# Performance work log

Measured on AMD Instinct MI355X. Metric: run time of the kernel, lower is better.

The kernel has to match this reference:

```python
import jax, jax.numpy as jnp
import numpy as np

N = 50000
D = 128
E = 600000


def setup_inputs() -> dict:
    key = jax.random.key(0)
    k1, k2, k3, k4, k5, k6 = jax.random.split(key, 6)
    x = jax.random.normal(k1, (N, D), dtype=jnp.float32)
    edge_index = jax.random.randint(k2, (2, E), 0, N, dtype=jnp.int32)
    s = 1.0 / np.sqrt(D)
    W1 = jax.random.uniform(k3, (D, D), dtype=jnp.float32, minval=-s, maxval=s)
    b1 = jax.random.uniform(k4, (D,), dtype=jnp.float32, minval=-s, maxval=s)
    W2 = jax.random.uniform(k5, (D, D), dtype=jnp.float32, minval=-s, maxval=s)
    b2 = jax.random.uniform(k6, (D,), dtype=jnp.float32, minval=-s, maxval=s)
    return {"x": x, "edge_index": edge_index, "W1": W1, "b1": b1, "W2": W2, "b2": b2}


def _gcn_conv(x, src, dst, W, b):
    # PyG GCNConv (default flow source->target): out[dst] += norm * (x @ W)[src] + b
    n = x.shape[0]
    deg = jax.ops.segment_sum(jnp.ones_like(dst, dtype=x.dtype), dst, num_segments=n)
    dinv = jnp.where(deg > 0, jax.lax.rsqrt(deg), 0.0)
    norm = dinv[src] * dinv[dst]          # [E+N]
    h = x @ W                             # [N, D]
    msg = h[src] * norm[:, None]          # [E+N, D] gather + scale
    out = jax.ops.segment_sum(msg, dst, num_segments=n)
    return out + b


def reference(x, edge_index, W1, b1, W2, b2):
    n = x.shape[0]
    loops = jnp.arange(n, dtype=edge_index.dtype)
    src = jnp.concatenate([edge_index[0], loops])  # add self-loops
    dst = jnp.concatenate([edge_index[1], loops])
    h = jax.nn.relu(_gcn_conv(x, src, dst, W1, b1))
    out = jax.nn.relu(_gcn_conv(h, src, dst, W2, b2))
    return out
```

## Files before the change

kernel.cpp:

```cpp
#include <hip/hip_runtime.h>
#include <stdint.h>

typedef __attribute__((ext_vector_type(8))) short bf16x8;
typedef __attribute__((ext_vector_type(4))) float f32x4;

#define CAP 64

__device__ __forceinline__ float bf2f(unsigned int u) {
    union { unsigned int i; float f; } v; v.i = u << 16; return v.f;
}
__device__ __forceinline__ unsigned int f2bf(float f) {
    union { float f; unsigned int i; } v; v.f = f;
    unsigned int b = v.i;
    b += 0x7FFFu + ((b >> 16) & 1u);
    return b >> 16;
}


__global__ void bucket_kernel(const int* __restrict__ src, const int* __restrict__ dst,
                              int* __restrict__ counts, unsigned short* __restrict__ bucket,
                              int E,
                              const float* __restrict__ W1, const float* __restrict__ W2,
                              unsigned short* __restrict__ Wt1, unsigned short* __restrict__ Wt2) {
    int t = blockIdx.x * 256 + threadIdx.x;
    if (t < 32768) {
        const float* W = (t < 16384) ? W1 : W2;
        unsigned short* O = (t < 16384) ? Wt1 : Wt2;
        int i = t & 16383;
        O[i] = (unsigned short)f2bf(W[(i & 127) * 128 + (i >> 7)]);
    }
    if (t < E) {
        int s = src[t], d = dst[t];
        int slot = atomicAdd(&counts[d], 1);
        if (slot < CAP - 1) bucket[(size_t)d * CAP + slot + 1] = (unsigned short)s;
    }
}


__global__ __launch_bounds__(256) void gemm128(const float* __restrict__ A,
                                               const unsigned short* __restrict__ Wt,
                                               const int* __restrict__ counts,
                                               unsigned short* __restrict__ bucket,
                                               unsigned short* __restrict__ G, int M) {
    int t = threadIdx.x;
    int wave = t >> 6, lane = t & 63;
    int mrow = lane & 15, quad = lane >> 4;

    {
        int row = blockIdx.x * 64 + (t >> 2);
        if (row < M) {
            int rows = 1 + min(counts[row], CAP - 1);
            int pe = (rows + 15) & ~15;
            if ((t & 3) == 0) bucket[(size_t)row * CAP] = (unsigned short)row;
            for (int idx = rows + (t & 3); idx < pe; idx += 4)
                bucket[(size_t)row * CAP + idx] = (unsigned short)M;
        }
    }
    if (blockIdx.x == 0 && t < 64)
        ((unsigned int*)G)[(size_t)M * 64 + t] = 0u;

    int m0 = (blockIdx.x * 4 + wave) * 16;
    int arow = m0 + mrow;
    int srow = arow < M ? arow : M - 1;
    const float* Arow = A + (size_t)srow * 128;

    f32x4 acc[8];
#pragma unroll
    for (int nt = 0; nt < 8; ++nt) acc[nt] = (f32x4){0.f, 0.f, 0.f, 0.f};

#pragma unroll
    for (int kb = 0; kb < 4; ++kb) {
        f32x4 lo = *(const f32x4*)(Arow + kb * 32 + quad * 8);
        f32x4 hi = *(const f32x4*)(Arow + kb * 32 + quad * 8 + 4);
        bf16x8 a;
#pragma unroll
        for (int i = 0; i < 4; ++i) { a[i] = (short)f2bf(lo[i]); a[i + 4] = (short)f2bf(hi[i]); }
#pragma unroll
        for (int nt = 0; nt < 8; ++nt) {
            bf16x8 b = *(const bf16x8*)(Wt + (size_t)(nt * 16 + mrow) * 128 + kb * 32 + quad * 8);
            acc[nt] = __builtin_amdgcn_mfma_f32_16x16x32_bf16(a, b, acc[nt], 0, 0, 0);
        }
    }

#pragma unroll
    for (int r = 0; r < 4; ++r) {
        int row = m0 + quad * 4 + r;
        if (row < M) {
            float dr = rsqrtf((float)counts[row] + 1.0f);
#pragma unroll
            for (int nt = 0; nt < 8; ++nt)
                G[(size_t)row * 128 + nt * 16 + mrow] = (unsigned short)f2bf(acc[nt][r] * dr);
        }
    }
}


template <bool FINAL>
__global__ __launch_bounds__(256) void agg_kernel(const unsigned short* __restrict__ g,
                                                  const int* __restrict__ counts,
                                                  const unsigned short* __restrict__ bucket,
                                                  const float* __restrict__ bias,
                                                  const unsigned short* __restrict__ Wt,
                                                  unsigned short* __restrict__ G2,
                                                  float* __restrict__ outf,
                                                  int N) {
    __shared__ __align__(16) unsigned short As[FINAL ? 1 : 16][136];
    int wave = threadIdx.x >> 6, lane = threadIdx.x & 63;
    int p = lane & 15, grp = lane >> 4;
    const char* gb = (const char*)g;
    int nb0 = blockIdx.x * 16 + wave * 4;

    if (!FINAL && blockIdx.x == 0 && threadIdx.x < 64)
        ((unsigned int*)G2)[(size_t)N * 64 + threadIdx.x] = 0u;

    float4 bva = ((const float4*)bias)[p * 2];
    float4 bvb = ((const float4*)bias)[p * 2 + 1];

    int degs[4]; unsigned int svs[4];
#pragma unroll
    for (int i = 0; i < 4; ++i) {
        int n = min(nb0 + i, N - 1);
        degs[i] = counts[n];
        svs[i]  = bucket[(size_t)n * CAP + lane];
    }

    uint4 vq[4][4];
#pragma unroll
    for (int i = 0; i < 4; ++i)
#pragma unroll
        for (int q = 0; q < 4; ++q) {
            int s = __shfl((int)svs[i], 4 * q + grp);
            vq[i][q] = *(const uint4*)(gb + (size_t)s * 256 + p * 16);
        }

#pragma unroll
    for (int i = 0; i < 4; ++i) {
        int deg = degs[i];
        int rows = 1 + min(deg, CAP - 1);
        int mr = (rows + 15) & ~15;
        float di = rsqrtf((float)deg + 1.0f);
        float acc[8];
#pragma unroll
        for (int k = 0; k < 8; ++k) acc[k] = 0.f;
#pragma unroll
        for (int q = 0; q < 4; ++q)
#pragma unroll
            for (int d = 0; d < 4; ++d) {
                unsigned int v = (&vq[i][q].x)[d];
                acc[d * 2]     += bf2f(v & 0xFFFFu);
                acc[d * 2 + 1] += bf2f(v >> 16);
            }
#pragma unroll 1
        for (int j0 = 16; j0 < mr; j0 += 16) {
            uint4 tq[4];
#pragma unroll
            for (int q = 0; q < 4; ++q) {
                int s = __shfl((int)svs[i], j0 + 4 * q + grp);
                tq[q] = *(const uint4*)(gb + (size_t)s * 256 + p * 16);
            }
#pragma unroll
            for (int q = 0; q < 4; ++q)
#pragma unroll
                for (int d = 0; d < 4; ++d) {
                    unsigned int v = (&tq[q].x)[d];
                    acc[d * 2]     += bf2f(v & 0xFFFFu);
                    acc[d * 2 + 1] += bf2f(v >> 16);
                }
        }
#pragma unroll
        for (int k = 0; k < 8; ++k) {
            acc[k] += __shfl_xor(acc[k], 16);
            acc[k] += __shfl_xor(acc[k], 32);
        }
        float o[8];
        o[0] = fmaxf(acc[0] * di + bva.x, 0.f);
        o[1] = fmaxf(acc[1] * di + bva.y, 0.f);
        o[2] = fmaxf(acc[2] * di + bva.z, 0.f);
        o[3] = fmaxf(acc[3] * di + bva.w, 0.f);
        o[4] = fmaxf(acc[4] * di + bvb.x, 0.f);
        o[5] = fmaxf(acc[5] * di + bvb.y, 0.f);
        o[6] = fmaxf(acc[6] * di + bvb.z, 0.f);
        o[7] = fmaxf(acc[7] * di + bvb.w, 0.f);

        if (FINAL) {
            if (grp == i) {
                int n = nb0 + i;
                if (n < N) {
                    float4* op = (float4*)(outf + (size_t)n * 128 + p * 8);
                    op[0] = make_float4(o[0], o[1], o[2], o[3]);
                    op[1] = make_float4(o[4], o[5], o[6], o[7]);
                }
            }
        } else {
            if (grp == i) {
                uint4 w;
                w.x = f2bf(o[0]) | (f2bf(o[1]) << 16);
                w.y = f2bf(o[2]) | (f2bf(o[3]) << 16);
                w.z = f2bf(o[4]) | (f2bf(o[5]) << 16);
                w.w = f2bf(o[6]) | (f2bf(o[7]) << 16);
                *(uint4*)&As[wave * 4 + i][p * 8] = w;
            }
        }
    }

    if (FINAL) return;

    __syncthreads();

    int mrow = lane & 15, quad = lane >> 4;
    f32x4 acc2[2];
    acc2[0] = (f32x4){0.f, 0.f, 0.f, 0.f};
    acc2[1] = (f32x4){0.f, 0.f, 0.f, 0.f};
#pragma unroll
    for (int kb = 0; kb < 4; ++kb) {
        bf16x8 a = *(const bf16x8*)(&As[mrow][kb * 32 + quad * 8]);
#pragma unroll
        for (int q = 0; q < 2; ++q) {
            int nt = wave * 2 + q;
            bf16x8 b = *(const bf16x8*)(Wt + (size_t)(nt * 16 + mrow) * 128 + kb * 32 + quad * 8);
            acc2[q] = __builtin_amdgcn_mfma_f32_16x16x32_bf16(a, b, acc2[q], 0, 0, 0);
        }
    }
#pragma unroll
    for (int r = 0; r < 4; ++r) {
        int row = blockIdx.x * 16 + quad * 4 + r;
        if (row < N) {
            float dr = rsqrtf((float)counts[row] + 1.0f);
#pragma unroll
            for (int q = 0; q < 2; ++q) {
                int nt = wave * 2 + q;
                G2[(size_t)row * 128 + nt * 16 + mrow] = (unsigned short)f2bf(acc2[q][r] * dr);
            }
        }
    }
}


extern "C" void kernel_launch(void* const* d_in, const int* in_sizes, int n_in,
                              void* d_out, int out_size, void* d_ws, size_t ws_size,
                              hipStream_t stream) {
    const float* x  = (const float*)d_in[0];
    const int*   ei = (const int*)d_in[1];
    const float* W1 = (const float*)d_in[2];
    const float* b1 = (const float*)d_in[3];
    const float* W2 = (const float*)d_in[4];
    const float* b2 = (const float*)d_in[5];
    float* out = (float*)d_out;

    int N = in_sizes[0] / 128;
    int E = in_sizes[1] / 2;
    const int* src = ei;
    const int* dst = ei + E;

    char* p = (char*)d_ws;
    auto alloc = [&](size_t bytes) {
        char* r = p; p += (bytes + 255) & ~(size_t)255; return r;
    };
    int*            counts = (int*)           alloc((size_t)N * 4);
    unsigned short* bucket = (unsigned short*)alloc((size_t)N * CAP * 2);
    unsigned short* g1     = (unsigned short*)alloc((size_t)(N + 1) * 128 * 2);
    unsigned short* g2     = (unsigned short*)alloc((size_t)(N + 1) * 128 * 2);
    unsigned short* Wt1    = (unsigned short*)alloc(16384 * 2);
    unsigned short* Wt2    = (unsigned short*)alloc(16384 * 2);

    hipMemsetAsync(counts, 0, (size_t)N * 4, stream);
    bucket_kernel<<<(E + 255) / 256, 256, 0, stream>>>(src, dst, counts, bucket, E,
                                                       W1, W2, Wt1, Wt2);

    gemm128<<<(N + 63) / 64, 256, 0, stream>>>(x, Wt1, counts, bucket, g1, N);
    agg_kernel<false><<<(N + 15) / 16, 256, 0, stream>>>(g1, counts, bucket, b1, Wt2, g2, nullptr, N);
    agg_kernel<true ><<<(N + 15) / 16, 256, 0, stream>>>(g2, counts, bucket, b2, nullptr, nullptr, out, N);
}
```

Before: 194.5 us.

## Replace global-atomic bucketing with range-partitioned LDS atomic bucket scan

Edge indices are first compacted to 16-bit arrays. Then 256 blocks each scan the whole compacted edge list and bucket only the destinations that fall in their own node range, using shared-memory atomics instead of global atomics. This removes the memset and the contended global atomics, and moves bucket padding out of the GEMM. In exchange every block rereads the full 1.2 MB destination array, which is 256 times the edge traffic, although most of it should hit in L2.

```diff
diff --git a/kernel.cpp b/kernel.cpp
--- a/kernel.cpp
+++ b/kernel.cpp
@@ -3,8 +3,10 @@
 
 typedef __attribute__((ext_vector_type(8))) short bf16x8;
 typedef __attribute__((ext_vector_type(4))) float f32x4;
+typedef __attribute__((ext_vector_type(8))) unsigned short u16x8;
 
 #define CAP 64
+#define SCAN_BLOCKS 256
 
 __device__ __forceinline__ float bf2f(unsigned int u) {
     union { unsigned int i; float f; } v; v.i = u << 16; return v.f;
@@ -17,11 +19,15 @@
 }
 
 
-__global__ void bucket_kernel(const int* __restrict__ src, const int* __restrict__ dst,
-                              int* __restrict__ counts, unsigned short* __restrict__ bucket,
-                              int E,
-                              const float* __restrict__ W1, const float* __restrict__ W2,
-                              unsigned short* __restrict__ Wt1, unsigned short* __restrict__ Wt2) {
+__global__ __launch_bounds__(256) void compact_kernel(const int* __restrict__ src,
+                                                      const int* __restrict__ dst,
+                                                      int E, int Epad,
+                                                      unsigned short* __restrict__ s16,
+                                                      unsigned short* __restrict__ d16,
+                                                      const float* __restrict__ W1,
+                                                      const float* __restrict__ W2,
+                                                      unsigned short* __restrict__ Wt1,
+                                                      unsigned short* __restrict__ Wt2) {
     int t = blockIdx.x * 256 + threadIdx.x;
     if (t < 32768) {
         const float* W = (t < 16384) ? W1 : W2;
@@ -29,10 +35,71 @@
         int i = t & 16383;
         O[i] = (unsigned short)f2bf(W[(i & 127) * 128 + (i >> 7)]);
     }
-    if (t < E) {
-        int s = src[t], d = dst[t];
-        int slot = atomicAdd(&counts[d], 1);
-        if (slot < CAP - 1) bucket[(size_t)d * CAP + slot + 1] = (unsigned short)s;
+    int e0 = t * 8;
+    if (e0 < Epad) {
+        u16x8 sv, dv;
+        if (e0 + 8 <= E) {
+            int4 a0 = *(const int4*)(src + e0), a1 = *(const int4*)(src + e0 + 4);
+            int4 b0 = *(const int4*)(dst + e0), b1 = *(const int4*)(dst + e0 + 4);
+            sv[0]=(unsigned short)a0.x; sv[1]=(unsigned short)a0.y; sv[2]=(unsigned short)a0.z; sv[3]=(unsigned short)a0.w;
+            sv[4]=(unsigned short)a1.x; sv[5]=(unsigned short)a1.y; sv[6]=(unsigned short)a1.z; sv[7]=(unsigned short)a1.w;
+            dv[0]=(unsigned short)b0.x; dv[1]=(unsigned short)b0.y; dv[2]=(unsigned short)b0.z; dv[3]=(unsigned short)b0.w;
+            dv[4]=(unsigned short)b1.x; dv[5]=(unsigned short)b1.y; dv[6]=(unsigned short)b1.z; dv[7]=(unsigned short)b1.w;
+        } else {
+#pragma unroll
+            for (int u = 0; u < 8; ++u) {
+                int e = e0 + u;
+                sv[u] = (e < E) ? (unsigned short)src[e] : (unsigned short)0xFFFF;
+                dv[u] = (e < E) ? (unsigned short)dst[e] : (unsigned short)0xFFFF;
+            }
+        }
+        *(u16x8*)(s16 + e0) = sv;
+        *(u16x8*)(d16 + e0) = dv;
+    }
+}
+
+
+__global__ __launch_bounds__(256) void bucket_scan(const unsigned short* __restrict__ s16,
+                                                   const unsigned short* __restrict__ d16,
+                                                   int Epad,
+                                                   int* __restrict__ counts,
+                                                   unsigned short* __restrict__ bucket,
+                                                   int N) {
+    __shared__ unsigned int cnt[512];
+    int tid = threadIdx.x;
+    int RANGE = (N + SCAN_BLOCKS - 1) / SCAN_BLOCKS;
+    int r0 = blockIdx.x * RANGE;
+    int rn = min(RANGE, N - r0);
+    if (rn <= 0) return;
+    for (int j = tid; j < RANGE; j += 256) cnt[j] = 0;
+    __syncthreads();
+
+#pragma unroll 1
+    for (int base = tid * 8; base < Epad; base += 256 * 8) {
+        u16x8 dv = *(const u16x8*)(d16 + base);
+#pragma unroll
+        for (int u = 0; u < 8; ++u) {
+            unsigned int rel = (unsigned int)dv[u] - (unsigned int)r0;
+            if (rel < (unsigned int)rn) {
+                unsigned int slot = atomicAdd(&cnt[rel], 1u);
+                if (slot < CAP - 1) {
+                    unsigned short s = s16[base + u];
+                    bucket[(size_t)dv[u] * CAP + slot + 1] = s;
+                }
+            }
+        }
+    }
+    __syncthreads();
+
+    for (int j = tid; j < rn; j += 256) {
+        int n = r0 + j;
+        int deg = (int)cnt[j];
+        counts[n] = deg;
+        bucket[(size_t)n * CAP] = (unsigned short)n;
+        int rows = 1 + min(deg, CAP - 1);
+        int pe = (rows + 15) & ~15;
+        for (int idx = rows; idx < pe; ++idx)
+            bucket[(size_t)n * CAP + idx] = (unsigned short)N;
     }
 }
 
@@ -40,22 +107,11 @@
 __global__ __launch_bounds__(256) void gemm128(const float* __restrict__ A,
                                                const unsigned short* __restrict__ Wt,
                                                const int* __restrict__ counts,
-                                               unsigned short* __restrict__ bucket,
                                                unsigned short* __restrict__ G, int M) {
     int t = threadIdx.x;
     int wave = t >> 6, lane = t & 63;
     int mrow = lane & 15, quad = lane >> 4;
 
-    {
-        int row = blockIdx.x * 64 + (t >> 2);
-        if (row < M) {
-            int rows = 1 + min(counts[row], CAP - 1);
-            int pe = (rows + 15) & ~15;
-            if ((t & 3) == 0) bucket[(size_t)row * CAP] = (unsigned short)row;
-            for (int idx = rows + (t & 3); idx < pe; idx += 4)
-                bucket[(size_t)row * CAP + idx] = (unsigned short)M;
-        }
-    }
     if (blockIdx.x == 0 && t < 64)
         ((unsigned int*)G)[(size_t)M * 64 + t] = 0u;
 
@@ -251,6 +307,7 @@
     int E = in_sizes[1] / 2;
     const int* src = ei;
     const int* dst = ei + E;
+    int Epad = (E + 2047) & ~2047;
 
     char* p = (char*)d_ws;
     auto alloc = [&](size_t bytes) {
@@ -262,12 +319,14 @@
     unsigned short* g2     = (unsigned short*)alloc((size_t)(N + 1) * 128 * 2);
     unsigned short* Wt1    = (unsigned short*)alloc(16384 * 2);
     unsigned short* Wt2    = (unsigned short*)alloc(16384 * 2);
-
-    hipMemsetAsync(counts, 0, (size_t)N * 4, stream);
-    bucket_kernel<<<(E + 255) / 256, 256, 0, stream>>>(src, dst, counts, bucket, E,
-                                                       W1, W2, Wt1, Wt2);
-
-    gemm128<<<(N + 63) / 64, 256, 0, stream>>>(x, Wt1, counts, bucket, g1, N);
+    unsigned short* s16    = (unsigned short*)alloc((size_t)Epad * 2);
+    unsigned short* d16    = (unsigned short*)alloc((size_t)Epad * 2);
+
+    int cblk = max((Epad / 8 + 255) / 256, 128);
+    compact_kernel<<<cblk, 256, 0, stream>>>(src, dst, E, Epad, s16, d16, W1, W2, Wt1, Wt2);
+    bucket_scan<<<SCAN_BLOCKS, 256, 0, stream>>>(s16, d16, Epad, counts, bucket, N);
+
+    gemm128<<<(N + 63) / 64, 256, 0, stream>>>(x, Wt1, counts, g1, N);
     agg_kernel<false><<<(N + 15) / 16, 256, 0, stream>>>(g1, counts, bucket, b1, Wt2, g2, nullptr, N);
     agg_kernel<true ><<<(N + 15) / 16, 256, 0, stream>>>(g2, counts, bucket, b2, nullptr, nullptr, out, N);
 }
```

Result: slower. 351.3 us (+80.6%).

## Replace global-atomic edge bucketing with two-pass range partition and LDS counting

Applied to the files above, without the earlier changes.

Edge bucketing now runs in two passes. The first pass partitions edges by dst>>8 into 256 coarse segments, using shared-memory histograms and one global atomic per range per block. The second pass has one block per range build the per-node buckets with LDS atomics, write the counts, and do the self-loop and padding fill that gemm128 used to do. This is meant to replace 600k scattered global atomics with local ones and drop the counts memset. In exchange it adds a kernel launch and a large segment buffer. Segments are capped at 4096 edges, which is enough for the expected ~3000 edges per range but silently drops edges if a range overflows. Packing src and dst into 16 bits each assumes N fits in 16 bits.

```diff
diff --git a/kernel.cpp b/kernel.cpp
--- a/kernel.cpp
+++ b/kernel.cpp
@@ -5,6 +5,7 @@
 typedef __attribute__((ext_vector_type(4))) float f32x4;
 
 #define CAP 64
+#define SEGCAP 4096
 
 __device__ __forceinline__ float bf2f(unsigned int u) {
     union { unsigned int i; float f; } v; v.i = u << 16; return v.f;
@@ -17,22 +18,101 @@
 }
 
 
-__global__ void bucket_kernel(const int* __restrict__ src, const int* __restrict__ dst,
-                              int* __restrict__ counts, unsigned short* __restrict__ bucket,
-                              int E,
-                              const float* __restrict__ W1, const float* __restrict__ W2,
-                              unsigned short* __restrict__ Wt1, unsigned short* __restrict__ Wt2) {
-    int t = blockIdx.x * 256 + threadIdx.x;
+__global__ __launch_bounds__(256) void partition_kernel(
+    const int* __restrict__ src, const int* __restrict__ dst, int E,
+    unsigned int* __restrict__ gcnt,
+    unsigned int* __restrict__ seg,
+    const float* __restrict__ W1, const float* __restrict__ W2,
+    unsigned short* __restrict__ Wt1, unsigned short* __restrict__ Wt2)
+{
+    __shared__ unsigned int hist[256];
+    int tid = threadIdx.x;
+    int t = blockIdx.x * 256 + tid;
+
     if (t < 32768) {
         const float* W = (t < 16384) ? W1 : W2;
         unsigned short* O = (t < 16384) ? Wt1 : Wt2;
         int i = t & 16383;
         O[i] = (unsigned short)f2bf(W[(i & 127) * 128 + (i >> 7)]);
     }
-    if (t < E) {
-        int s = src[t], d = dst[t];
-        int slot = atomicAdd(&counts[d], 1);
-        if (slot < CAP - 1) bucket[(size_t)d * CAP + slot + 1] = (unsigned short)s;
+
+    hist[tid] = 0;
+    __syncthreads();
+
+    int e0 = blockIdx.x * 2048 + tid * 8;
+    unsigned int pair[8]; int rng[8]; bool val[8];
+    if (e0 + 8 <= E) {
+        int4 a0 = *(const int4*)(src + e0), a1 = *(const int4*)(src + e0 + 4);
+        int4 b0 = *(const int4*)(dst + e0), b1 = *(const int4*)(dst + e0 + 4);
+        int sa[8] = {a0.x,a0.y,a0.z,a0.w,a1.x,a1.y,a1.z,a1.w};
+        int da[8] = {b0.x,b0.y,b0.z,b0.w,b1.x,b1.y,b1.z,b1.w};
+#pragma unroll
+        for (int u = 0; u < 8; ++u) {
+            pair[u] = ((unsigned int)da[u] << 16) | (unsigned int)sa[u];
+            rng[u] = da[u] >> 8; val[u] = true;
+        }
+    } else {
+#pragma unroll
+        for (int u = 0; u < 8; ++u) {
+            int e = e0 + u;
+            val[u] = (e < E);
+            int s = val[u] ? src[e] : 0, d = val[u] ? dst[e] : 0;
+            pair[u] = ((unsigned int)d << 16) | (unsigned int)s;
+            rng[u] = d >> 8;
+        }
+    }
+
+#pragma unroll
+    for (int u = 0; u < 8; ++u)
+        if (val[u]) atomicAdd(&hist[rng[u]], 1u);
+    __syncthreads();
+
+    {
+        unsigned int c = hist[tid];
+        if (c) hist[tid] = atomicAdd(&gcnt[tid], c);
+    }
+    __syncthreads();
+
+#pragma unroll
+    for (int u = 0; u < 8; ++u)
+        if (val[u]) {
+            unsigned int pos = atomicAdd(&hist[rng[u]], 1u);
+            if (pos < SEGCAP) seg[(size_t)rng[u] * SEGCAP + pos] = pair[u];
+        }
+}
+
+
+__global__ __launch_bounds__(256) void bucket_build(
+    const unsigned int* __restrict__ gcnt,
+    const unsigned int* __restrict__ seg,
+    int* __restrict__ counts, unsigned short* __restrict__ bucket, int N)
+{
+    __shared__ unsigned int cnt[256];
+    int r = blockIdx.x, tid = threadIdx.x;
+    cnt[tid] = 0;
+    __syncthreads();
+
+    int er = min((int)gcnt[r], SEGCAP);
+    const unsigned int* s = seg + (size_t)r * SEGCAP;
+#pragma unroll 1
+    for (int i = tid; i < er; i += 256) {
+        unsigned int pr = s[i];
+        int d = pr >> 16;
+        int slot = (int)atomicAdd(&cnt[d & 255], 1u);
+        if (slot < CAP - 1)
+            bucket[(size_t)d * CAP + slot + 1] = (unsigned short)(pr & 0xFFFFu);
+    }
+    __syncthreads();
+
+    int n = r * 256 + tid;
+    if (n < N) {
+        int deg = (int)cnt[tid];
+        counts[n] = deg;
+        bucket[(size_t)n * CAP] = (unsigned short)n;
+        int rows = 1 + min(deg, CAP - 1);
+        int pe = (rows + 15) & ~15;
+        for (int idx = rows; idx < pe; ++idx)
+            bucket[(size_t)n * CAP + idx] = (unsigned short)N;
     }
 }
 
@@ -40,22 +120,11 @@
 __global__ __launch_bounds__(256) void gemm128(const float* __restrict__ A,
                                                const unsigned short* __restrict__ Wt,
                                                const int* __restrict__ counts,
-                                               unsigned short* __restrict__ bucket,
                                                unsigned short* __restrict__ G, int M) {
     int t = threadIdx.x;
     int wave = t >> 6, lane = t & 63;
     int mrow = lane & 15, quad = lane >> 4;
 
-    {
-        int row = blockIdx.x * 64 + (t >> 2);
-        if (row < M) {
-            int rows = 1 + min(counts[row], CAP - 1);
-            int pe = (rows + 15) & ~15;
-            if ((t & 3) == 0) bucket[(size_t)row * CAP] = (unsigned short)row;
-            for (int idx = rows + (t & 3); idx < pe; idx += 4)
-                bucket[(size_t)row * CAP + idx] = (unsigned short)M;
-        }
-    }
     if (blockIdx.x == 0 && t < 64)
         ((unsigned int*)G)[(size_t)M * 64 + t] = 0u;
 
@@ -251,6 +320,7 @@
     int E = in_sizes[1] / 2;
     const int* src = ei;
     const int* dst = ei + E;
+    int NR = (N + 255) >> 8;
 
     char* p = (char*)d_ws;
     auto alloc = [&](size_t bytes) {
@@ -262,12 +332,17 @@
     unsigned short* g2     = (unsigned short*)alloc((size_t)(N + 1) * 128 * 2);
     unsigned short* Wt1    = (unsigned short*)alloc(16384 * 2);
     unsigned short* Wt2    = (unsigned short*)alloc(16384 * 2);
-
-    hipMemsetAsync(counts, 0, (size_t)N * 4, stream);
-    bucket_kernel<<<(E + 255) / 256, 256, 0, stream>>>(src, dst, counts, bucket, E,
-                                                       W1, W2, Wt1, Wt2);
-
-    gemm128<<<(N + 63) / 64, 256, 0, stream>>>(x, Wt1, counts, bucket, g1, N);
+    unsigned int*   gcnt   = (unsigned int*)  alloc(256 * 4);
+    unsigned int*   seg    = (unsigned int*)  alloc((size_t)256 * SEGCAP * 4);
+
+    hipMemsetAsync(gcnt, 0, 256 * 4, stream);
+
+    int ablk = (E + 2047) / 2048;
+    if (ablk < 128) ablk = 128;
+    partition_kernel<<<ablk, 256, 0, stream>>>(src, dst, E, gcnt, seg, W1, W2, Wt1, Wt2);
+    bucket_build<<<NR, 256, 0, stream>>>(gcnt, seg, counts, bucket, N);
+
+    gemm128<<<(N + 63) / 64, 256, 0, stream>>>(x, Wt1, counts, g1, N);
     agg_kernel<false><<<(N + 15) / 16, 256, 0, stream>>>(g1, counts, bucket, b1, Wt2, g2, nullptr, N);
     agg_kernel<true ><<<(N + 15) / 16, 256, 0, stream>>>(g2, counts, bucket, b2, nullptr, nullptr, out, N);
 }
```

Measured after the change: 179.8 us, median of 2. 7.5% less time.
